# Performance work log

Hardware: AMD Instinct MI355X
Metric: run time of the kernel (lower is better)

## Reference

```python
import jax, jax.numpy as jnp
import numpy as np

GROUP = 4
BN_EPS = 1e-5


def setup_inputs() -> dict:
    key = jax.random.key(0)
    ks = jax.random.split(key, 6)
    B, C, N = 8, 64, 4096
    K, KS, OUT = 20, 20, 64
    feature = jax.random.normal(ks[0], (B, C, N), dtype=jnp.float32)
    neigh_indexs = jax.random.randint(ks[1], (B * N, K), 0, B * N, dtype=jnp.int64)
    permatrix = jax.random.normal(ks[2], (B * N, K, KS), dtype=jnp.float32)
    conv_w = jax.random.normal(ks[3], (OUT, C), dtype=jnp.float32) * (1.0 / np.sqrt(C))
    conv_b = jax.random.normal(ks[4], (OUT,), dtype=jnp.float32) * 0.01
    bn_w = jnp.ones((OUT,), dtype=jnp.float32)
    bn_b = jnp.zeros((OUT,), dtype=jnp.float32)
    return {"feature": feature, "neigh_indexs": neigh_indexs, "permatrix": permatrix,
            "conv_w": conv_w, "conv_b": conv_b, "bn_w": bn_w, "bn_b": bn_b}


def reference(feature, neigh_indexs, permatrix, conv_w, conv_b, bn_w, bn_b):
    B, C, N = feature.shape
    BN = B * N
    K = neigh_indexs.shape[1]
    # flatten points: [B, C, N] -> [B*N, C]
    flat = jnp.transpose(feature, (0, 2, 1)).reshape(BN, C)
    # irregular neighbor gather: [B*N, k, C] -> [B*N, C, k]
    feats = jnp.transpose(flat[neigh_indexs], (0, 2, 1))
    # group channel shuffle (num_feat > 3 path)
    feats = feats.reshape(BN, GROUP, C // GROUP, K)
    feats = jnp.transpose(feats, (0, 2, 1, 3)).reshape(BN, C, K)
    # per-point soft-permutation matmul: [B*N, C, kernel_size]
    feats = jnp.einsum('nck,nks->ncs', feats, permatrix)
    # conv1x1 (in_c -> out_c) then max over kernel_size
    out = jnp.einsum('ncs,oc->nos', feats, conv_w) + conv_b[None, :, None]
    out = jnp.max(out, axis=-1)  # [B*N, out_c]
    out = jnp.transpose(out.reshape(B, N, -1), (0, 2, 1))  # [B, out_c, N]
    # BatchNorm1d (training-mode batch statistics over batch+points)
    mean = jnp.mean(out, axis=(0, 2), keepdims=True)
    var = jnp.var(out, axis=(0, 2), keepdims=True)
    out = (out - mean) * jax.lax.rsqrt(var + BN_EPS)
    return out * bn_w[None, :, None] + bn_b[None, :, None]
```

## Files before the change

### kernel.cpp

```cpp
#include <hip/hip_runtime.h>

#define C_IN 64
#define N_PT 4096
#define BN_TOT 32768
#define KNB 20
#define KSZ 20
#define C_OUT 64
#define BN_EPS 1e-5f
#define PPB 16

__global__ __launch_bounds__(512) void k1_gemm(const float* __restrict__ feat,
                                               const float* __restrict__ conv_w,
                                               float* __restrict__ G,
                                               float* __restrict__ sums) {
    __shared__ float fl[C_IN * 64];
    __shared__ float wl[C_IN * C_OUT];
    const int b  = blockIdx.x >> 6;
    const int n0 = (blockIdx.x & 63) << 6;
    const int t  = threadIdx.x;

    if (blockIdx.x == 0 && t < 132) sums[t] = 0.f;

    const float4* fsrc = reinterpret_cast<const float4*>(
        feat + (size_t)b * C_IN * N_PT + n0);
    float4* fl4 = reinterpret_cast<float4*>(fl);
#pragma unroll
    for (int j = 0; j < 2; ++j) {
        int idx = j * 512 + t;
        int c = idx >> 4, p4 = idx & 15;
        fl4[idx] = fsrc[c * (N_PT / 4) + p4];
    }
#pragma unroll
    for (int j = 0; j < 8; ++j) {
        int i = j * 512 + t;
        int o = i >> 6, co = i & 63;
        int cn = ((co & 3) << 4) | (co >> 2);
        wl[cn * 64 + o] = conv_w[i];
    }
    __syncthreads();

    const int lane = t & 63;
    const int ob = (t >> 6) << 3;

    float acc[8];
#pragma unroll
    for (int j = 0; j < 8; ++j) acc[j] = 0.f;

#pragma unroll 4
    for (int c = 0; c < C_IN; ++c) {
        float fc = fl[c * 64 + lane];
        float4 w0 = *reinterpret_cast<const float4*>(&wl[c * 64 + ob]);
        float4 w1 = *reinterpret_cast<const float4*>(&wl[c * 64 + ob + 4]);
        acc[0] += fc * w0.x; acc[1] += fc * w0.y;
        acc[2] += fc * w0.z; acc[3] += fc * w0.w;
        acc[4] += fc * w1.x; acc[5] += fc * w1.y;
        acc[6] += fc * w1.z; acc[7] += fc * w1.w;
    }

    size_t m = (size_t)b * N_PT + n0 + lane;
    float4* gdst = reinterpret_cast<float4*>(G + m * 64 + ob);
    gdst[0] = make_float4(acc[0], acc[1], acc[2], acc[3]);
    gdst[1] = make_float4(acc[4], acc[5], acc[6], acc[7]);
}

__global__ __launch_bounds__(256) void k2_main(
        const int* __restrict__ nidx,
        const float* __restrict__ P,
        const float* __restrict__ G,
        const float* __restrict__ conv_b,
        float* __restrict__ omax,
        float* __restrict__ sums,
        unsigned* __restrict__ ctr,
        const float* __restrict__ bn_w,
        const float* __restrict__ bn_b,
        float* __restrict__ ss) {
    __shared__ float Pl[PPB * KNB * KSZ];
    __shared__ int   Il[PPB * KNB];
    const int t = threadIdx.x;
    const int base = blockIdx.x * PPB;

    const float4* ps = reinterpret_cast<const float4*>(P + (size_t)base * (KNB * KSZ));
    float4* pd = reinterpret_cast<float4*>(Pl);
#pragma unroll
    for (int j = 0; j < 6; ++j) pd[j * 256 + t] = ps[j * 256 + t];
    if (t < 64) pd[1536 + t] = ps[1536 + t];
    if (t < 80)
        reinterpret_cast<int4*>(Il)[t] =
            reinterpret_cast<const int4*>(nidx + (size_t)base * KNB)[t];
    __syncthreads();

    const int lane = t & 63;
    const int wid = t >> 6;
    const int p0 = wid * 4;
    const float cb = conv_b[lane];
    float ls = 0.f, ls2 = 0.f;

    float g[2][KNB];

#pragma unroll
    for (int k = 0; k < KNB; ++k)
        g[0][k] = G[(size_t)Il[p0 * KNB + k] * 64 + lane];

#pragma unroll
    for (int i = 0; i < 4; ++i) {
        const int cur = i & 1;

        if (i < 3) {
#pragma unroll
            for (int k = 0; k < KNB; ++k)
                g[cur ^ 1][k] = G[(size_t)Il[(p0 + i + 1) * KNB + k] * 64 + lane];
        }

        float acc[KSZ];
#pragma unroll
        for (int s = 0; s < KSZ; ++s) acc[s] = 0.f;

        const float* pp = Pl + (p0 + i) * (KNB * KSZ);
#pragma unroll
        for (int k = 0; k < KNB; ++k) {
#pragma unroll
            for (int s4 = 0; s4 < 5; ++s4) {
                float4 pv = *reinterpret_cast<const float4*>(&pp[k * KSZ + s4 * 4]);
                acc[s4 * 4 + 0] += g[cur][k] * pv.x;
                acc[s4 * 4 + 1] += g[cur][k] * pv.y;
                acc[s4 * 4 + 2] += g[cur][k] * pv.z;
                acc[s4 * 4 + 3] += g[cur][k] * pv.w;
            }
        }

        float mx = acc[0];
#pragma unroll
        for (int s = 1; s < KSZ; ++s) mx = fmaxf(mx, acc[s]);
        mx += cb;
        omax[(size_t)(base + p0 + i) * 64 + lane] = mx;
        ls += mx;
        ls2 += mx * mx;
    }

    __syncthreads();
    float* r1 = Pl;
    float* r2 = Pl + 256;
    r1[wid * 64 + lane] = ls;
    r2[wid * 64 + lane] = ls2;
    __syncthreads();
    if (wid == 0) {
        float a  = r1[lane] + r1[64 + lane] + r1[128 + lane] + r1[192 + lane];
        float c2 = r2[lane] + r2[64 + lane] + r2[128 + lane] + r2[192 + lane];
        atomicAdd(&sums[lane], a);
        atomicAdd(&sums[64 + lane], c2);
    }
    __syncthreads();

    __shared__ bool lastBlk;
    if (t == 0) {
        __threadfence();
        lastBlk = (atomicAdd(ctr, 1u) == (unsigned)(gridDim.x - 1));
    }
    __syncthreads();
    if (lastBlk && t < 64) {
        float s1 = atomicAdd(&sums[t], 0.f);
        float s2 = atomicAdd(&sums[64 + t], 0.f);
        const float inv = 1.f / (float)BN_TOT;
        float mean = s1 * inv;
        float var  = s2 * inv - mean * mean;
        float rstd = rsqrtf(var + BN_EPS);
        float sc = rstd * bn_w[t];
        ss[t] = sc;
        ss[64 + t] = bn_b[t] - mean * sc;
    }
}

__global__ __launch_bounds__(512) void k4_apply(const float* __restrict__ omax,
                                                const float* __restrict__ ss,
                                                float* __restrict__ out) {
    const int b  = blockIdx.x >> 6;
    const int n0 = (blockIdx.x & 63) << 6;
    const int t  = threadIdx.x;
    const int nl = t & 63;
    const int ob = (t >> 6) << 3;

    const size_t m = (size_t)b * N_PT + n0 + nl;
    const float4* src = reinterpret_cast<const float4*>(omax + m * 64 + ob);
    float v[8];
    float4 x0 = src[0], x1 = src[1];
    v[0] = x0.x; v[1] = x0.y; v[2] = x0.z; v[3] = x0.w;
    v[4] = x1.x; v[5] = x1.y; v[6] = x1.z; v[7] = x1.w;
#pragma unroll
    for (int j = 0; j < 8; ++j) {
        int o = ob + j;
        float sc = ss[o];
        float sh = ss[64 + o];
        out[(size_t)b * C_OUT * N_PT + (size_t)o * N_PT + n0 + nl] =
            v[j] * sc + sh;
    }
}

extern "C" void kernel_launch(void* const* d_in, const int* in_sizes, int n_in,
                              void* d_out, int out_size, void* d_ws, size_t ws_size,
                              hipStream_t stream) {
    const float* feature = (const float*)d_in[0];
    const int*   nidx    = (const int*)d_in[1];
    const float* perm    = (const float*)d_in[2];
    const float* conv_w  = (const float*)d_in[3];
    const float* conv_b  = (const float*)d_in[4];
    const float* bn_w    = (const float*)d_in[5];
    const float* bn_b    = (const float*)d_in[6];
    float* out = (float*)d_out;

    char* ws = (char*)d_ws;
    float* G    = (float*)ws;
    float* OM   = (float*)(ws + (size_t)8 * 1024 * 1024);
    float* SUMS = (float*)(ws + (size_t)16 * 1024 * 1024);
    unsigned* CTR = (unsigned*)(SUMS + 128);
    float* SS   = SUMS + 132;

    k1_gemm<<<512, 512, 0, stream>>>(feature, conv_w, G, SUMS);
    k2_main<<<BN_TOT / PPB, 256, 0, stream>>>(nidx, perm, G, conv_b, OM, SUMS,
                                              CTR, bn_w, bn_b, SS);
    k4_apply<<<512, 512, 0, stream>>>(OM, SS, out);
}
```

Baseline: 206.1 us.

## Stage permatrix via direct global-to-LDS loads and read indices with scalar loads

The main kernel now copies the permatrix tile with global_load_lds, which writes directly into LDS instead of going through registers. It drops the LDS staging of neighbour indices and reads them through wave-uniform (readfirstlane) addresses, so they can become scalar loads. Columns 8-19 of each point's matrix are read straight from global memory with uniform addresses, splitting operand traffic between LDS and the scalar cache. The first GEMM kernel is retiled to 256-thread blocks covering 32 points each, and the inner loop unroll is reduced. The cost is a second read of part of the permatrix through the cache path, plus reliance on correct synchronisation of the async LDS loads.

New measurement: 303.4 us. +47.2%, slower.

```diff
diff --git a/kernel.cpp b/kernel.cpp
--- a/kernel.cpp
+++ b/kernel.cpp
@@ -1,4 +1,5 @@
 #include <hip/hip_runtime.h>
+#include <stdint.h>
 
 #define C_IN 64
 #define N_PT 4096
@@ -8,15 +9,24 @@
 #define C_OUT 64
 #define BN_EPS 1e-5f
 #define PPB 16
-
-__global__ __launch_bounds__(512) void k1_gemm(const float* __restrict__ feat,
+#define PELEM (KNB * KSZ)
+
+typedef __attribute__((address_space(3))) uint32_t* lds_ptr_t;
+typedef const __attribute__((address_space(1))) uint32_t* gl_ptr_t;
+
+__device__ __forceinline__ void glds16(const float* gp, float* lp) {
+    __builtin_amdgcn_global_load_lds((gl_ptr_t)(const void*)gp,
+                                     (lds_ptr_t)(void*)lp, 16, 0, 0);
+}
+
+__global__ __launch_bounds__(256) void k1_gemm(const float* __restrict__ feat,
                                                const float* __restrict__ conv_w,
                                                float* __restrict__ G,
                                                float* __restrict__ sums) {
-    __shared__ float fl[C_IN * 64];
+    __shared__ float fl[C_IN * 32];
     __shared__ float wl[C_IN * C_OUT];
-    const int b  = blockIdx.x >> 6;
-    const int n0 = (blockIdx.x & 63) << 6;
+    const int b  = blockIdx.x >> 7;
+    const int n0 = (blockIdx.x & 127) << 5;
     const int t  = threadIdx.x;
 
     if (blockIdx.x == 0 && t < 132) sums[t] = 0.f;
@@ -26,13 +36,13 @@
     float4* fl4 = reinterpret_cast<float4*>(fl);
 #pragma unroll
     for (int j = 0; j < 2; ++j) {
-        int idx = j * 512 + t;
-        int c = idx >> 4, p4 = idx & 15;
+        int idx = j * 256 + t;
+        int c = idx >> 3, p4 = idx & 7;
         fl4[idx] = fsrc[c * (N_PT / 4) + p4];
     }
 #pragma unroll
-    for (int j = 0; j < 8; ++j) {
-        int i = j * 512 + t;
+    for (int j = 0; j < 16; ++j) {
+        int i = j * 256 + t;
         int o = i >> 6, co = i & 63;
         int cn = ((co & 3) << 4) | (co >> 2);
         wl[cn * 64 + o] = conv_w[i];
@@ -40,7 +50,9 @@
     __syncthreads();
 
     const int lane = t & 63;
-    const int ob = (t >> 6) << 3;
+    const int wid  = t >> 6;
+    const int p    = lane & 31;
+    const int ob   = wid * 16 + (lane >> 5) * 8;
 
     float acc[8];
 #pragma unroll
@@ -48,7 +60,7 @@
 
 #pragma unroll 4
     for (int c = 0; c < C_IN; ++c) {
-        float fc = fl[c * 64 + lane];
+        float fc = fl[c * 32 + p];
         float4 w0 = *reinterpret_cast<const float4*>(&wl[c * 64 + ob]);
         float4 w1 = *reinterpret_cast<const float4*>(&wl[c * 64 + ob + 4]);
         acc[0] += fc * w0.x; acc[1] += fc * w0.y;
@@ -57,7 +69,7 @@
         acc[6] += fc * w1.z; acc[7] += fc * w1.w;
     }
 
-    size_t m = (size_t)b * N_PT + n0 + lane;
+    size_t m = (size_t)b * N_PT + n0 + p;
     float4* gdst = reinterpret_cast<float4*>(G + m * 64 + ob);
     gdst[0] = make_float4(acc[0], acc[1], acc[2], acc[3]);
     gdst[1] = make_float4(acc[4], acc[5], acc[6], acc[7]);
@@ -74,65 +86,75 @@
         const float* __restrict__ bn_w,
         const float* __restrict__ bn_b,
         float* __restrict__ ss) {
-    __shared__ float Pl[PPB * KNB * KSZ];
-    __shared__ int   Il[PPB * KNB];
-    const int t = threadIdx.x;
-    const int base = blockIdx.x * PPB;
-
-    const float4* ps = reinterpret_cast<const float4*>(P + (size_t)base * (KNB * KSZ));
-    float4* pd = reinterpret_cast<float4*>(Pl);
-#pragma unroll
-    for (int j = 0; j < 6; ++j) pd[j * 256 + t] = ps[j * 256 + t];
-    if (t < 64) pd[1536 + t] = ps[1536 + t];
-    if (t < 80)
-        reinterpret_cast<int4*>(Il)[t] =
-            reinterpret_cast<const int4*>(nidx + (size_t)base * KNB)[t];
-    __syncthreads();
-
+    __shared__ float Pl[PPB * PELEM];
+    const int t    = threadIdx.x;
     const int lane = t & 63;
-    const int wid = t >> 6;
-    const int p0 = wid * 4;
+    const int wid  = t >> 6;
+    const int tile = blockIdx.x;
+
+    const float* Pg = P + (size_t)tile * (PPB * PELEM);
+    for (int i = wid; i < 25; i += 4)
+        glds16(Pg + i * 256 + lane * 4, &Pl[i * 256]);
+    __syncthreads();
+
     const float cb = conv_b[lane];
+    const int pbase = wid * 4;
     float ls = 0.f, ls2 = 0.f;
 
     float g[2][KNB];
-
-#pragma unroll
-    for (int k = 0; k < KNB; ++k)
-        g[0][k] = G[(size_t)Il[p0 * KNB + k] * 64 + lane];
-
-#pragma unroll
-    for (int i = 0; i < 4; ++i) {
-        const int cur = i & 1;
-
-        if (i < 3) {
+    {
+        const int n0 = __builtin_amdgcn_readfirstlane(tile * PPB + pbase);
+        const int* ip = nidx + (size_t)n0 * KNB;
+#pragma unroll
+        for (int k = 0; k < KNB; ++k)
+            g[0][k] = G[(size_t)ip[k] * 64 + lane];
+    }
+
+#pragma unroll
+    for (int j = 0; j < 4; ++j) {
+        const int cur = j & 1;
+
+        if (j < 3) {
+            const int nn = __builtin_amdgcn_readfirstlane(tile * PPB + pbase + j + 1);
+            const int* ip = nidx + (size_t)nn * KNB;
 #pragma unroll
             for (int k = 0; k < KNB; ++k)
-                g[cur ^ 1][k] = G[(size_t)Il[(p0 + i + 1) * KNB + k] * 64 + lane];
+                g[cur ^ 1][k] = G[(size_t)ip[k] * 64 + lane];
         }
 
+        const int n = __builtin_amdgcn_readfirstlane(tile * PPB + pbase + j);
+        const float* pl = Pl + (pbase + j) * PELEM;
+        const float* pg = P + (size_t)n * PELEM;
+
         float acc[KSZ];
 #pragma unroll
         for (int s = 0; s < KSZ; ++s) acc[s] = 0.f;
 
-        const float* pp = Pl + (p0 + i) * (KNB * KSZ);
-#pragma unroll
+#pragma unroll 4
         for (int k = 0; k < KNB; ++k) {
-#pragma unroll
-            for (int s4 = 0; s4 < 5; ++s4) {
-                float4 pv = *reinterpret_cast<const float4*>(&pp[k * KSZ + s4 * 4]);
-                acc[s4 * 4 + 0] += g[cur][k] * pv.x;
-                acc[s4 * 4 + 1] += g[cur][k] * pv.y;
-                acc[s4 * 4 + 2] += g[cur][k] * pv.z;
-                acc[s4 * 4 + 3] += g[cur][k] * pv.w;
-            }
+            const float gk = g[cur][k];
+            float4 a  = *reinterpret_cast<const float4*>(pl + k * KSZ);
+            float4 bb = *reinterpret_cast<const float4*>(pl + k * KSZ + 4);
+            float4 c0 = *reinterpret_cast<const float4*>(pg + k * KSZ + 8);
+            float4 c1 = *reinterpret_cast<const float4*>(pg + k * KSZ + 12);
+            float4 c2 = *reinterpret_cast<const float4*>(pg + k * KSZ + 16);
+            acc[0]  += gk * a.x;  acc[1]  += gk * a.y;
+            acc[2]  += gk * a.z;  acc[3]  += gk * a.w;
+            acc[4]  += gk * bb.x; acc[5]  += gk * bb.y;
+            acc[6]  += gk * bb.z; acc[7]  += gk * bb.w;
+            acc[8]  += gk * c0.x; acc[9]  += gk * c0.y;
+            acc[10] += gk * c0.z; acc[11] += gk * c0.w;
+            acc[12] += gk * c1.x; acc[13] += gk * c1.y;
+            acc[14] += gk * c1.z; acc[15] += gk * c1.w;
+            acc[16] += gk * c2.x; acc[17] += gk * c2.y;
+            acc[18] += gk * c2.z; acc[19] += gk * c2.w;
         }
 
         float mx = acc[0];
 #pragma unroll
         for (int s = 1; s < KSZ; ++s) mx = fmaxf(mx, acc[s]);
         mx += cb;
-        omax[(size_t)(base + p0 + i) * 64 + lane] = mx;
+        omax[(size_t)n * 64 + lane] = mx;
         ls += mx;
         ls2 += mx * mx;
     }
@@ -214,7 +236,7 @@
     unsigned* CTR = (unsigned*)(SUMS + 128);
     float* SS   = SUMS + 132;
 
-    k1_gemm<<<512, 512, 0, stream>>>(feature, conv_w, G, SUMS);
+    k1_gemm<<<1024, 256, 0, stream>>>(feature, conv_w, G, SUMS);
     k2_main<<<BN_TOT / PPB, 256, 0, stream>>>(nidx, perm, G, conv_b, OM, SUMS,
                                               CTR, bn_w, bn_b, SS);
     k4_apply<<<512, 512, 0, stream>>>(OM, SS, out);
```
